# Performance work log

Measured on AMD Instinct MI355X. Metric: run time of the kernel, lower is better.

## Reference

```python
import jax, jax.numpy as jnp
import numpy as np

ENC_HID = 512
DEC_HID = 512


def setup_inputs() -> dict:
    key = jax.random.key(0)
    k1, k2, k3, k4, k5 = jax.random.split(key, 5)
    hidden = jax.random.normal(k1, (64, DEC_HID), dtype=jnp.float32)
    encoder_outputs = jax.random.normal(k2, (1024, 64, 2 * ENC_HID), dtype=jnp.float32)
    in_dim = 2 * ENC_HID + DEC_HID
    # Linear params (stored as [in, out] for x @ W + b)
    scale = 1.0 / np.sqrt(in_dim)
    W = jax.random.uniform(k3, (in_dim, DEC_HID), dtype=jnp.float32, minval=-scale, maxval=scale)
    b = jax.random.uniform(k4, (DEC_HID,), dtype=jnp.float32, minval=-scale, maxval=scale)
    v = jax.random.uniform(k5, (DEC_HID,), dtype=jnp.float32)  # torch.rand in [0,1)
    return {"hidden": hidden, "encoder_outputs": encoder_outputs, "W": W, "b": b, "v": v}


def reference(hidden, encoder_outputs, W, b, v):
    # hidden: [B, Dd]; encoder_outputs: [S, B, 2*De]
    src_len = encoder_outputs.shape[0]
    enc = jnp.transpose(encoder_outputs, (1, 0, 2))            # [B, S, 2*De]
    hid = jnp.broadcast_to(hidden[:, None, :], (hidden.shape[0], src_len, hidden.shape[1]))  # [B, S, Dd]
    concat = jnp.concatenate([hid, enc], axis=2)               # [B, S, Dd+2*De]
    energy = jnp.tanh(concat @ W + b)                          # [B, S, Dd]
    scores = jnp.einsum("bsd,d->bs", energy, v)                # [B, S]
    return jax.nn.softmax(scores, axis=1)
```

## Files before the change

kernel.cpp:

```cpp
#include <hip/hip_runtime.h>
#include <stdint.h>


typedef float  floatx4 __attribute__((ext_vector_type(4)));
typedef float  floatx8 __attribute__((ext_vector_type(8)));
typedef __bf16 bf16x8  __attribute__((ext_vector_type(8)));
typedef short  short8  __attribute__((ext_vector_type(8)));

union bfu { bf16x8 v; short8 s; };

#define LOG2E_X2 2.8853900817779268f

__device__ __forceinline__ void async_ld16(const void* g, void* l) {
  __builtin_amdgcn_global_load_lds(
      (const __attribute__((address_space(1))) void*)g,
      (__attribute__((address_space(3))) void*)l, 16, 0, 0);
}

__global__ void wt_convert(const float* __restrict__ W, __bf16* __restrict__ Wt) {
  __shared__ float tile[64][65];
  const int kt = blockIdx.x >> 3;
  const int nt = blockIdx.x & 7;
  const int c  = threadIdx.x & 63;
  const int r4 = threadIdx.x >> 6;
  #pragma unroll 4
  for (int i = 0; i < 16; i++) {
    int r = i * 4 + r4;
    tile[r][c] = W[(long)(512 + kt * 64 + r) * 512 + nt * 64 + c];
  }
  __syncthreads();
  #pragma unroll 4
  for (int i = 0; i < 16; i++) {
    int n = i * 4 + r4;
    Wt[(long)(nt * 64 + n) * 1024 + kt * 64 + c] = (__bf16)tile[c][n];
  }
}

__global__ void hproj_kernel(const float* __restrict__ hidden,
                             const float* __restrict__ W,
                             const float* __restrict__ bias,
                             float* __restrict__ hproj) {
  const int tid = threadIdx.x;
  const int b_  = blockIdx.x >> 2;
  const int kc  = blockIdx.x & 3;
  __shared__ float hid[128];
  if (tid < 128) hid[tid] = hidden[b_ * 512 + kc * 128 + tid];
  __syncthreads();
  float acc = (kc == 0) ? bias[tid] : 0.f;
  const float* Wp = W + (long)(kc * 128) * 512 + tid;
  #pragma unroll 8
  for (int k = 0; k < 128; k++) acc = fmaf(hid[k], Wp[(long)k * 512], acc);
  atomicAdd(&hproj[b_ * 512 + tid], acc);
}

__global__ __launch_bounds__(256, 2) void gemm_score(
    const float* __restrict__ enc,
    const __bf16* __restrict__ Wt,
    const float* __restrict__ hproj,
    const float* __restrict__ v,
    float* __restrict__ scores)
{
  __shared__ float ldsA0[2048];
  __shared__ float ldsA1[2048];
  __shared__ float bscore[64];

  const int tid  = threadIdx.x;
  const int lane = tid & 63;
  const int wv   = tid >> 6;
  const int q    = lane >> 4;
  const int t    = lane & 15;
  const long m0  = (long)blockIdx.x * 64;

  const __bf16* bp = Wt + (long)(wv * 128 + t) * 1024 + q * 8;

  if (tid < 64) bscore[tid] = 0.f;

  floatx4 acc[4][8];
  #pragma unroll
  for (int i = 0; i < 4; i++)
    #pragma unroll
    for (int j = 0; j < 8; j++)
      acc[i][j] = (floatx4){0.f, 0.f, 0.f, 0.f};

  auto issueA = [&](int kk, float* buf) {
    #pragma unroll
    for (int i = 0; i < 2; i++) {
      int idx = i * 256 + tid;
      int c = idx >> 7, m = (idx >> 1) & 63, h = idx & 1;
      async_ld16(enc + (m0 + m) * 1024 + kk + c * 8 + h * 4, buf + idx * 4);
    }
  };
  auto loadB = [&](int kk, short8* br) {
    #pragma unroll
    for (int ct = 0; ct < 8; ct++) {
      union bfu u;
      u.v = *(const bf16x8*)(bp + kk + ct * 16 * 1024);
      br[ct] = u.s;
    }
  };
  auto fragA = [&](const float* buf, short8* af) {
    #pragma unroll
    for (int rt = 0; rt < 4; rt++) {
      floatx8 av = *(const floatx8*)(buf + (q * 128 + (rt * 16 + t) * 2) * 4);
      union bfu u;
      #pragma unroll
      for (int j = 0; j < 8; j++) u.v[j] = (__bf16)av[j];
      af[rt] = u.s;
    }
  };
  auto domfma = [&](short8* af, short8* br) {
    #pragma unroll
    for (int rt = 0; rt < 4; rt++)
      #pragma unroll
      for (int ct = 0; ct < 8; ct++)
        acc[rt][ct] = __builtin_amdgcn_mfma_f32_16x16x32_bf16(
            af[rt], br[ct], acc[rt][ct], 0, 0, 0);
  };

  short8 b0[8], b1[8], afr[4];

  issueA(0, ldsA0);
  loadB(0, b0);
  __syncthreads();

  for (int T = 0; T < 16; T++) {
    const int kk = T * 64;
    issueA(kk + 32, ldsA1);
    loadB(kk + 32, b1);
    fragA(ldsA0, afr);
    domfma(afr, b0);
    __syncthreads();

    if (T < 15) {
      issueA(kk + 64, ldsA0);
      loadB(kk + 64, b0);
    }
    fragA(ldsA1, afr);
    domfma(afr, b1);
    __syncthreads();
  }

  float vv[8];
  #pragma unroll
  for (int ct = 0; ct < 8; ct++) vv[ct] = v[wv * 128 + ct * 16 + t];

  #pragma unroll
  for (int rt = 0; rt < 4; rt++) {
    #pragma unroll
    for (int r = 0; r < 4; r++) {
      int row = rt * 16 + q * 4 + r;
      const float* hrow = hproj + row * 512 + wv * 128 + t;
      float s = 0.f;
      #pragma unroll
      for (int ct = 0; ct < 8; ct++) {
        float e  = acc[rt][ct][r] + hrow[ct * 16];
        float ex = __builtin_amdgcn_exp2f(e * LOG2E_X2);
        float th = 1.f - 2.f * __builtin_amdgcn_rcpf(ex + 1.f);
        s = fmaf(vv[ct], th, s);
      }
      s += __shfl_xor(s, 1);
      s += __shfl_xor(s, 2);
      s += __shfl_xor(s, 4);
      s += __shfl_xor(s, 8);
      if (t == 0) atomicAdd(&bscore[row], s);
    }
  }
  __syncthreads();
  if (tid < 64) scores[(long)tid * 1024 + blockIdx.x] = bscore[tid];
}

__global__ void softmax_kernel(const float* __restrict__ scores,
                               float* __restrict__ out) {
  const int b_   = blockIdx.x;
  const int tid  = threadIdx.x;
  const int lane = tid & 63;
  const int wv   = tid >> 6;
  __shared__ float redmax[4], redsum[4];

  float x[4];
  #pragma unroll
  for (int i = 0; i < 4; i++) x[i] = scores[b_ * 1024 + i * 256 + tid];
  float mx = fmaxf(fmaxf(x[0], x[1]), fmaxf(x[2], x[3]));
  #pragma unroll
  for (int off = 1; off < 64; off <<= 1) mx = fmaxf(mx, __shfl_xor(mx, off));
  if (lane == 0) redmax[wv] = mx;
  __syncthreads();
  mx = fmaxf(fmaxf(redmax[0], redmax[1]), fmaxf(redmax[2], redmax[3]));

  float e[4], s = 0.f;
  #pragma unroll
  for (int i = 0; i < 4; i++) { e[i] = __expf(x[i] - mx); s += e[i]; }
  #pragma unroll
  for (int off = 1; off < 64; off <<= 1) s += __shfl_xor(s, off);
  if (lane == 0) redsum[wv] = s;
  __syncthreads();
  s = redsum[0] + redsum[1] + redsum[2] + redsum[3];
  float inv = 1.f / s;
  #pragma unroll
  for (int i = 0; i < 4; i++) out[b_ * 1024 + i * 256 + tid] = e[i] * inv;
}

extern "C" void kernel_launch(void* const* d_in, const int* in_sizes, int n_in,
                              void* d_out, int out_size, void* d_ws, size_t ws_size,
                              hipStream_t stream) {
  (void)in_sizes; (void)n_in; (void)out_size; (void)ws_size;
  const float* hidden = (const float*)d_in[0];
  const float* enc    = (const float*)d_in[1];
  const float* W      = (const float*)d_in[2];
  const float* bias   = (const float*)d_in[3];
  const float* v      = (const float*)d_in[4];
  float* out = (float*)d_out;

  char* ws = (char*)d_ws;
  __bf16* Wt    = (__bf16*)ws;
  float*  hproj = (float*)(ws + (1 << 20));
  float*  scores= (float*)(ws + (1 << 20) + (128 << 10));

  hipMemsetAsync(hproj, 0, 64 * 512 * sizeof(float), stream);
  wt_convert<<<128, 256, 0, stream>>>(W, Wt);
  hproj_kernel<<<256, 512, 0, stream>>>(hidden, W, bias, hproj);
  gemm_score<<<1024, 256, 0, stream>>>(enc, Wt, hproj, v, scores);
  softmax_kernel<<<64, 256, 0, stream>>>(scores, out);
}
```

Baseline: 491.8 us.

## Load A tiles directly from global into registers, dropping LDS staging and barriers

The GEMM kernel no longer stages encoder-output tiles in LDS through async global-to-LDS loads. Each wave now loads its own A fragments straight into registers, double-buffered in registers, and interleaves the B loads with the MFMA loop. This removes the per-iteration __syncthreads and the LDS round trip. In exchange, all four waves now load the same A rows from global memory (about 4x redundant A traffic, relying on L2/L1 hits), and register pressure rises.

After: 559.8 us. +13.8%, slower.

```diff
diff --git a/kernel.cpp b/kernel.cpp
--- a/kernel.cpp
+++ b/kernel.cpp
@@ -10,12 +10,6 @@
 union bfu { bf16x8 v; short8 s; };
 
 #define LOG2E_X2 2.8853900817779268f
-
-__device__ __forceinline__ void async_ld16(const void* g, void* l) {
-  __builtin_amdgcn_global_load_lds(
-      (const __attribute__((address_space(1))) void*)g,
-      (__attribute__((address_space(3))) void*)l, 16, 0, 0);
-}
 
 __global__ void wt_convert(const float* __restrict__ W, __bf16* __restrict__ Wt) {
   __shared__ float tile[64][65];
@@ -60,8 +54,6 @@
     const float* __restrict__ v,
     float* __restrict__ scores)
 {
-  __shared__ float ldsA0[2048];
-  __shared__ float ldsA1[2048];
   __shared__ float bscore[64];
 
   const int tid  = threadIdx.x;
@@ -71,9 +63,16 @@
   const int t    = lane & 15;
   const long m0  = (long)blockIdx.x * 64;
 
-  const __bf16* bp = Wt + (long)(wv * 128 + t) * 1024 + q * 8;
-
   if (tid < 64) bscore[tid] = 0.f;
+
+  const float* aptr[4];
+  #pragma unroll
+  for (int rt = 0; rt < 4; rt++)
+    aptr[rt] = enc + (m0 + rt * 16 + t) * 1024 + q * 8;
+  const __bf16* bptr[8];
+  #pragma unroll
+  for (int ct = 0; ct < 8; ct++)
+    bptr[ct] = Wt + (long)(wv * 128 + ct * 16 + t) * 1024 + q * 8;
 
   floatx4 acc[4][8];
   #pragma unroll
@@ -82,63 +81,58 @@
     for (int j = 0; j < 8; j++)
       acc[i][j] = (floatx4){0.f, 0.f, 0.f, 0.f};
 
-  auto issueA = [&](int kk, float* buf) {
-    #pragma unroll
-    for (int i = 0; i < 2; i++) {
-      int idx = i * 256 + tid;
-      int c = idx >> 7, m = (idx >> 1) & 63, h = idx & 1;
-      async_ld16(enc + (m0 + m) * 1024 + kk + c * 8 + h * 4, buf + idx * 4);
-    }
+  auto loadA = [&](int kk, floatx8* ar) {
+    #pragma unroll
+    for (int rt = 0; rt < 4; rt++) ar[rt] = *(const floatx8*)(aptr[rt] + kk);
   };
-  auto loadB = [&](int kk, short8* br) {
-    #pragma unroll
-    for (int ct = 0; ct < 8; ct++) {
+  auto cvtA = [&](const floatx8* ar, short8* af) {
+    #pragma unroll
+    for (int rt = 0; rt < 4; rt++) {
       union bfu u;
-      u.v = *(const bf16x8*)(bp + kk + ct * 16 * 1024);
-      br[ct] = u.s;
+      #pragma unroll
+      for (int j = 0; j < 8; j++) u.v[j] = (__bf16)ar[rt][j];
+      af[rt] = u.s;
     }
   };
-  auto fragA = [&](const float* buf, short8* af) {
-    #pragma unroll
-    for (int rt = 0; rt < 4; rt++) {
-      floatx8 av = *(const floatx8*)(buf + (q * 128 + (rt * 16 + t) * 2) * 4);
-      union bfu u;
-      #pragma unroll
-      for (int j = 0; j < 8; j++) u.v[j] = (__bf16)av[j];
-      af[rt] = u.s;
-    }
-  };
-  auto domfma = [&](short8* af, short8* br) {
-    #pragma unroll
-    for (int rt = 0; rt < 4; rt++)
-      #pragma unroll
-      for (int ct = 0; ct < 8; ct++)
-        acc[rt][ct] = __builtin_amdgcn_mfma_f32_16x16x32_bf16(
-            af[rt], br[ct], acc[rt][ct], 0, 0, 0);
-  };
-
-  short8 b0[8], b1[8], afr[4];
-
-  issueA(0, ldsA0);
-  loadB(0, b0);
-  __syncthreads();
+
+  floatx8 ar[4];
+  short8  b0[8], b1[8], af[4];
+
+  loadA(0, ar);
+  #pragma unroll
+  for (int ct = 0; ct < 8; ct++) {
+    union bfu u; u.v = *(const bf16x8*)(bptr[ct]); b0[ct] = u.s;
+  }
 
   for (int T = 0; T < 16; T++) {
     const int kk = T * 64;
-    issueA(kk + 32, ldsA1);
-    loadB(kk + 32, b1);
-    fragA(ldsA0, afr);
-    domfma(afr, b0);
-    __syncthreads();
-
-    if (T < 15) {
-      issueA(kk + 64, ldsA0);
-      loadB(kk + 64, b0);
-    }
-    fragA(ldsA1, afr);
-    domfma(afr, b1);
-    __syncthreads();
-  }
+
+    cvtA(ar, af);
+    loadA(kk + 32, ar);
+    #pragma unroll
+    for (int ct = 0; ct < 8; ct++) {
+      #pragma unroll
+      for (int rt = 0; rt < 4; rt++)
+        acc[rt][ct] = __builtin_amdgcn_mfma_f32_16x16x32_bf16(
+            af[rt], b0[ct], acc[rt][ct], 0, 0, 0);
+      union bfu u; u.v = *(const bf16x8*)(bptr[ct] + kk + 32); b1[ct] = u.s;
+    }
+
+    cvtA(ar, af);
+    if (T < 15) loadA(kk + 64, ar);
+    #pragma unroll
+    for (int ct = 0; ct < 8; ct++) {
+      #pragma unroll
+      for (int rt = 0; rt < 4; rt++)
+        acc[rt][ct] = __builtin_amdgcn_mfma_f32_16x16x32_bf16(
+            af[rt], b1[ct], acc[rt][ct], 0, 0, 0);
+      if (T < 15) {
+        union bfu u; u.v = *(const bf16x8*)(bptr[ct] + kk + 64); b0[ct] = u.s;
+      }
+    }
+  }
+
+  __syncthreads();
 
   float vv[8];
   #pragma unroll
```
